# Performance work log

Measured on AMD Instinct MI355X. Metric: run time of the kernel, lower is better.

Reference implementation:

```python
import jax, jax.numpy as jnp
import numpy as np

B, S, DIN, DQ, DK = 4, 2048, 1024, 64, 64
NEG_INF = -jnp.inf


def _make_mask(sq, sk):
    # Mirrors createMask: causal mask (-inf where key_idx > query_idx),
    # except 3 randomly chosen (row, col) 'global token' pairs left at 0.
    # torch version uses random.sample; we use a fixed numpy RNG for determinism.
    rng = np.random.default_rng(0)
    g_rows = rng.choice(sk, 3, replace=False)  # sampled from range(lrlen)
    g_cols = rng.choice(sq, 3, replace=False)  # sampled from range(sequence_len)
    row = jnp.arange(sq)[:, None]
    col = jnp.arange(sk)[None, :]
    mask = jnp.where(col > row, NEG_INF, 0.0).astype(jnp.float32)
    mask = mask.at[jnp.asarray(g_rows), jnp.asarray(g_cols)].set(0.0)
    return mask  # [sq, sk]


def setup_inputs() -> dict:
    key = jax.random.key(0)
    ks = jax.random.split(key, 9)
    sc = 1.0 / np.sqrt(DIN)
    return {
        "q": jax.random.normal(ks[0], (B, S, DIN), jnp.float32),
        "k": jax.random.normal(ks[1], (B, S, DIN), jnp.float32),
        "v": jax.random.normal(ks[2], (B, S, DIN), jnp.float32),
        "Wq": jax.random.normal(ks[3], (DIN, DQ), jnp.float32) * sc,
        "bq": jax.random.normal(ks[4], (DQ,), jnp.float32) * sc,
        "Wk": jax.random.normal(ks[5], (DIN, DK), jnp.float32) * sc,
        "bk": jax.random.normal(ks[6], (DK,), jnp.float32) * sc,
        "Wv": jax.random.normal(ks[7], (DIN, DK), jnp.float32) * sc,
        "bv": jax.random.normal(ks[8], (DK,), jnp.float32) * sc,
    }


def reference(q, k, v, Wq, bq, Wk, bk, Wv, bv):
    Q = q @ Wq + bq            # [B,S,DQ]
    K = k @ Wk + bk            # [B,S,DK]
    V = v @ Wv + bv            # [B,S,DK]
    scores = jnp.einsum("bqd,bkd->bqk", Q, K)  # [B,S,S]
    mask = _make_mask(scores.shape[-2], scores.shape[-1])
    denom = jnp.asarray(K.shape[-1], jnp.float32) ** 0.5
    # NOTE: original adds mask BEFORE dividing by sqrt(d_k); -inf survives division.
    attn = jax.nn.softmax((scores + mask) / denom, axis=-1)
    return jnp.einsum("bqk,bkd->bqd", attn, V)  # [B,S,DK]
```

## Files before the change

### kernel.cpp

```cpp
#include <hip/hip_runtime.h>
#include <cstdint>
#include <cstddef>
#include <math.h>

#define SEQ    2048
#define NBATCH 4
#define DIN    1024
#define DH     64

typedef __attribute__((ext_vector_type(8))) short  short8;
typedef __attribute__((ext_vector_type(4))) float  floatx4;
typedef __attribute__((ext_vector_type(4))) unsigned short ushort4v;

#define MFMA16(a, b, c) __builtin_amdgcn_mfma_f32_16x16x32_bf16((a), (b), (c), 0, 0, 0)

__device__ __forceinline__ unsigned short f2bf(float x) {
  unsigned u = __float_as_uint(x);
  return (unsigned short)((u + 0x8000u) >> 16);
}
__device__ __forceinline__ float bf2f(unsigned short h) {
  return __uint_as_float(((unsigned)h) << 16);
}

namespace nprng {

struct PCG64 {
  __uint128_t state, inc;
  bool has_uint32;
  uint32_t uinteger;
};

static inline void pcg_step(PCG64 &g) {
  const __uint128_t MULT =
      (((__uint128_t)0x2360ed051fc65da4ULL) << 64) | 0x4385df649fccf645ULL;
  g.state = g.state * MULT + g.inc;
}

static inline uint64_t pcg_output(const PCG64 &g) {
  uint64_t hi = (uint64_t)(g.state >> 64);
  uint64_t lo = (uint64_t)g.state;
  uint64_t x = hi ^ lo;
  unsigned rot = (unsigned)(g.state >> 122) & 63u;
  return (x >> rot) | (x << ((64u - rot) & 63u));
}

static inline uint64_t pcg_next64(PCG64 &g) { pcg_step(g); return pcg_output(g); }

static inline uint32_t pcg_next32(PCG64 &g) {
  if (g.has_uint32) { g.has_uint32 = false; return g.uinteger; }
  uint64_t n = pcg_next64(g);
  g.has_uint32 = true;
  g.uinteger = (uint32_t)(n >> 32);
  return (uint32_t)(n & 0xffffffffu);
}

static inline void pcg_seed_from_seedseq0(PCG64 &g) {
  const uint32_t MULT_A = 0x931e8875u;
  const uint32_t MULT_B = 0x58f38dedu;
  const uint32_t MIX_L  = 0xca01f9ddu;
  const uint32_t MIX_R  = 0x4973f715u;
  uint32_t hc = 0x43b0d7e5u;
  uint32_t pool[4];
  for (int i = 0; i < 4; i++) {
    uint32_t v = 0u;
    v ^= hc; hc *= MULT_A; v *= hc; v ^= v >> 16;
    pool[i] = v;
  }
  for (int is = 0; is < 4; is++) {
    for (int id = 0; id < 4; id++) {
      if (is == id) continue;
      uint32_t h = pool[is];
      h ^= hc; hc *= MULT_A; h *= hc; h ^= h >> 16;
      uint32_t r = (pool[id] * MIX_L) ^ (h * MIX_R);
      r ^= r >> 16;
      pool[id] = r;
    }
  }
  uint32_t hb = 0x8b51f9ddu;
  uint32_t w[8];
  for (int i = 0; i < 8; i++) {
    uint32_t v = pool[i & 3];
    v ^= hb; hb *= MULT_B; v *= hb; v ^= v >> 16;
    w[i] = v;
  }
  uint64_t sv[4];
  for (int k = 0; k < 4; k++)
    sv[k] = (uint64_t)w[2 * k] | ((uint64_t)w[2 * k + 1] << 32);
  __uint128_t initstate = (((__uint128_t)sv[0]) << 64) | sv[1];
  __uint128_t initseq   = (((__uint128_t)sv[2]) << 64) | sv[3];
  g.state = 0; g.inc = (initseq << 1) | 1;
  pcg_step(g);
  g.state += initstate;
  pcg_step(g);
  g.has_uint32 = false; g.uinteger = 0;
}

static inline uint32_t bounded32(PCG64 &g, uint32_t rng ) {
  if (rng == 0) return 0;
  const uint32_t rng_excl = rng + 1u;
  uint64_t m = (uint64_t)pcg_next32(g) * (uint64_t)rng_excl;
  uint32_t leftover = (uint32_t)m;
  if (leftover < rng_excl) {
    const uint32_t threshold = (uint32_t)(0xffffffffu - rng) % rng_excl;
    while (leftover < threshold) {
      m = (uint64_t)pcg_next32(g) * (uint64_t)rng_excl;
      leftover = (uint32_t)m;
    }
  }
  return (uint32_t)(m >> 32);
}

static inline void choice3_2048(PCG64 &g, long long idx[3]) {
  const int pop = 2048, sz = 3;
  uint64_t hs[4] = { (uint64_t)-1, (uint64_t)-1, (uint64_t)-1, (uint64_t)-1 };
  const uint64_t mask = 3;
  for (int j = pop - sz; j < pop; j++) {
    uint64_t val = (uint64_t)bounded32(g, (uint32_t)j);
    uint64_t loc = val & mask;
    while (hs[loc] != (uint64_t)-1 && hs[loc] != val) loc = (loc + 1) & mask;
    if (hs[loc] == (uint64_t)-1) {
      hs[loc] = val;
      idx[j - pop + sz] = (long long)val;
    } else {
      loc = (uint64_t)j & mask;
      while (hs[loc] != (uint64_t)-1) loc = (loc + 1) & mask;
      hs[loc] = (uint64_t)j;
      idx[j - pop + sz] = (long long)j;
    }
  }
  for (int i = 2; i >= 1; i--) {
    uint32_t j = bounded32(g, (uint32_t)i);
    long long t = idx[j]; idx[j] = idx[i]; idx[i] = t;
  }
}

}

__global__ __launch_bounds__(256) void wtrans_kernel(
    const float* __restrict__ Wq, const float* __restrict__ Wk,
    const float* __restrict__ Wv, unsigned short* __restrict__ WT) {
  int idx = blockIdx.x * 256 + threadIdx.x;
  int p   = idx >> 16;
  int rem = idx & 65535;
  int n   = rem >> 10;
  int k   = rem & 1023;
  const float* W = (p == 0) ? Wq : (p == 1) ? Wk : Wv;
  WT[idx] = f2bf(W[k * 64 + n]);
}

__global__ __launch_bounds__(256, 3) void proj_kernel(
    const float* __restrict__ xq, const float* __restrict__ xk,
    const float* __restrict__ xv, const unsigned short* __restrict__ WT,
    const float* __restrict__ bq, const float* __restrict__ bk,
    const float* __restrict__ bv,
    unsigned short* __restrict__ QP, unsigned short* __restrict__ KP,
    unsigned short* __restrict__ VPT) {
  const int proj = blockIdx.y;
  const float* X    = (proj == 0) ? xq : (proj == 1) ? xk : xv;
  const float* bias = (proj == 0) ? bq : (proj == 1) ? bk : bv;

  const int m0   = blockIdx.x * 32;
  const int tid  = threadIdx.x;
  const int w    = tid >> 6;
  const int l    = tid & 63;
  const int quad = l >> 4;
  const int lx   = l & 15;

  __shared__ unsigned short Xs[32][264];
  __shared__ float Cs[32][68];

  const float* Xg = X + (size_t)m0 * DIN;
  const unsigned short* Wrow = WT + (size_t)proj * 65536 + (size_t)(w * 16 + lx) * 1024 + quad * 8;

  float4 xg[8];
  short8 wc[8], wn[8];

#pragma unroll
  for (int i = 0; i < 8; i++)
    xg[i] = *(const float4*)(Xg + (size_t)(4 * i + w) * DIN + l * 4);
#pragma unroll
  for (int ks = 0; ks < 8; ks++)
    wc[ks] = *(const short8*)(Wrow + ks * 32);

  floatx4 acc0 = {0.f, 0.f, 0.f, 0.f}, acc1 = acc0;

#pragma unroll
  for (int c = 0; c < 4; c++) {
#pragma unroll
    for (int i = 0; i < 8; i++) {
      ushort4v v;
      v[0] = f2bf(xg[i].x); v[1] = f2bf(xg[i].y);
      v[2] = f2bf(xg[i].z); v[3] = f2bf(xg[i].w);
      *(ushort4v*)&Xs[4 * i + w][l * 4] = v;
    }
    if (c < 3) {
      const int k0n = (c + 1) * 256;
#pragma unroll
      for (int i = 0; i < 8; i++)
        xg[i] = *(const float4*)(Xg + (size_t)(4 * i + w) * DIN + k0n + l * 4);
#pragma unroll
      for (int ks = 0; ks < 8; ks++)
        wn[ks] = *(const short8*)(Wrow + k0n + ks * 32);
    }
    __syncthreads();

#pragma unroll
    for (int ks = 0; ks < 8; ks++) {
      const short8 a0 = *(const short8*)&Xs[lx][ks * 32 + quad * 8];
      const short8 a1 = *(const short8*)&Xs[16 + lx][ks * 32 + quad * 8];
      acc0 = MFMA16(a0, wc[ks], acc0);
      acc1 = MFMA16(a1, wc[ks], acc1);
    }
    __syncthreads();

    if (c < 3) {
#pragma unroll
      for (int ks = 0; ks < 8; ks++) wc[ks] = wn[ks];
    }
  }

  const float bb = bias[w * 16 + lx];
#pragma unroll
  for (int i = 0; i < 4; i++) {
    Cs[quad * 4 + i][w * 16 + lx]      = acc0[i] + bb;
    Cs[16 + quad * 4 + i][w * 16 + lx] = acc1[i] + bb;
  }
  __syncthreads();

  if (proj < 2) {
    unsigned short* outp = (proj == 0) ? QP : KP;
    const int row = tid >> 3;
    const int d0  = (tid & 7) * 8;
    short8 v;
#pragma unroll
    for (int j = 0; j < 8; j++) v[j] = (short)f2bf(Cs[row][d0 + j]);
    *(short8*)(outp + (size_t)(m0 + row) * 64 + d0) = v;
  } else {
    const int dim = tid >> 2;
    const int s0  = (tid & 3) * 8;
    const int bq_ = m0 >> 11;
    const int sq  = (m0 & 2047) + s0;
    short8 v;
#pragma unroll
    for (int j = 0; j < 8; j++) v[j] = (short)f2bf(Cs[s0 + j][dim]);
    *(short8*)(VPT + ((size_t)bq_ * 64 + dim) * SEQ + sq) = v;
  }
}

__global__ __launch_bounds__(256, 2) void attn_kernel(
    const unsigned short* __restrict__ QP, const unsigned short* __restrict__ KP,
    const unsigned short* __restrict__ VPT, float* __restrict__ out,
    int R0, int C0, int R1, int C1, int R2, int C2) {
  const int b    = blockIdx.y;
  const int bx   = blockIdx.x;
  const int qi   = (bx & 1) ? (127 - (bx >> 1)) : (bx >> 1);
  const int q0   = qi * 16;
  const int tid  = threadIdx.x;
  const int w    = tid >> 6;
  const int l    = tid & 63;
  const int quad = l >> 4;
  const int lx   = l & 15;

  __shared__ unsigned short Ps[4][16][72];
  __shared__ float Os[4][16][64];
  __shared__ float mS[4][16], lS[4][16];
  __shared__ float lgS[3];
  __shared__ int   lgF[3];

  const unsigned short* Qb = QP + ((size_t)b * SEQ + q0) * 64;
  const unsigned short* Kb = KP + (size_t)b * SEQ * 64;
  const unsigned short* Vb = VPT + (size_t)b * 64 * SEQ;

  const short8 aq0 = *(const short8*)(Qb + (size_t)lx * 64 + quad * 8);
  const short8 aq1 = *(const short8*)(Qb + (size_t)lx * 64 + 32 + quad * 8);

  floatx4 O[4];
  float m_i[4], l_i[4];
#pragma unroll
  for (int c = 0; c < 4; c++) O[c] = (floatx4){0.f, 0.f, 0.f, 0.f};
#pragma unroll
  for (int i = 0; i < 4; i++) { m_i[i] = -INFINITY; l_i[i] = 0.f; }

  const int T = (q0 + 79) >> 6;

  for (int t = w; t < T; t += 4) {
    const int k0 = t << 6;
    const bool mT = (t == T - 1);

    short8 kf[8], vf[8];
#pragma unroll
    for (int c = 0; c < 4; c++) {
#pragma unroll
      for (int s = 0; s < 2; s++) {
        kf[c * 2 + s] = *(const short8*)(Kb + (size_t)(k0 + 16 * c + lx) * 64 + s * 32 + quad * 8);
        vf[s * 4 + c] = *(const short8*)(Vb + (size_t)(16 * c + lx) * SEQ + k0 + s * 32 + quad * 8);
      }
    }

    floatx4 sc[4];
#pragma unroll
    for (int c = 0; c < 4; c++) {
      sc[c] = (floatx4){0.f, 0.f, 0.f, 0.f};
      sc[c] = MFMA16(aq0, kf[2 * c], sc[c]);
      sc[c] = MFMA16(aq1, kf[2 * c + 1], sc[c]);
    }

    float mt[4], al[4];
#pragma unroll
    for (int i = 0; i < 4; i++) {
      const int rowg = q0 + quad * 4 + i;
      float vmax = -INFINITY;
#pragma unroll
      for (int c = 0; c < 4; c++) {
        float v = sc[c][i] * 0.125f;
        if (mT && (k0 + 16 * c + lx) > rowg) v = -INFINITY;
        sc[c][i] = v;
        vmax = fmaxf(vmax, v);
      }
      mt[i] = vmax;
    }
#pragma unroll
    for (int i = 0; i < 4; i++) {
#pragma unroll
      for (int off = 8; off >= 1; off >>= 1)
        mt[i] = fmaxf(mt[i], __shfl_xor(mt[i], off));
      const float mn = fmaxf(m_i[i], mt[i]);
      al[i] = __expf(m_i[i] - mn);
      m_i[i] = mn;
      float s = 0.f;
#pragma unroll
      for (int c = 0; c < 4; c++) {
        float p = __expf(sc[c][i] - mn);
        Ps[w][quad * 4 + i][16 * c + lx] = f2bf(p);
        s += p;
      }
#pragma unroll
      for (int off = 8; off >= 1; off >>= 1) s += __shfl_xor(s, off);
      l_i[i] = l_i[i] * al[i] + s;
    }
#pragma unroll
    for (int c = 0; c < 4; c++)
#pragma unroll
      for (int i = 0; i < 4; i++) O[c][i] *= al[i];
    asm volatile("" ::: "memory");
    const short8 pf0 = *(const short8*)&Ps[w][lx][quad * 8];
    const short8 pf1 = *(const short8*)&Ps[w][lx][32 + quad * 8];
#pragma unroll
    for (int c = 0; c < 4; c++) {
      O[c] = MFMA16(pf0, vf[c],     O[c]);
      O[c] = MFMA16(pf1, vf[4 + c], O[c]);
    }
  }

  if (lx == 0) {
#pragma unroll
    for (int i = 0; i < 4; i++) {
      mS[w][quad * 4 + i] = m_i[i];
      lS[w][quad * 4 + i] = l_i[i];
    }
  }
#pragma unroll
  for (int c = 0; c < 4; c++)
#pragma unroll
    for (int i = 0; i < 4; i++) Os[w][quad * 4 + i][16 * c + lx] = O[c][i];

  if (w == 0) {
#pragma unroll
    for (int p = 0; p < 3; p++) {
      const int R = (p == 0) ? R0 : (p == 1) ? R1 : R2;
      const int C = (p == 0) ? C0 : (p == 1) ? C1 : C2;
      const int act = (R >= q0 && R < q0 + 16 && C > R);
      float d = 0.f;
      if (act) {
        const float qv = bf2f(QP[((size_t)b * SEQ + R) * 64 + l]);
        const float kv = bf2f(KP[((size_t)b * SEQ + C) * 64 + l]);
        d = qv * kv;
#pragma unroll
        for (int off = 32; off >= 1; off >>= 1) d += __shfl_xor(d, off);
        d *= 0.125f;
      }
      if (l == 0) { lgF[p] = act; lgS[p] = d; }
    }
  }
  __syncthreads();

  {
    const int row = tid >> 4;
    const int d0  = (tid & 15) * 4;
    const int Rs[3] = {R0, R1, R2};
    const int Cs3[3] = {C0, C1, C2};

    float mf = -INFINITY;
#pragma unroll
    for (int w4 = 0; w4 < 4; w4++) mf = fmaxf(mf, mS[w4][row]);
#pragma unroll
    for (int p = 0; p < 3; p++)
      if (lgF[p] && (Rs[p] - q0) == row) mf = fmaxf(mf, lgS[p]);

    float lf = 0.f;
    float o0 = 0.f, o1 = 0.f, o2 = 0.f, o3 = 0.f;
#pragma unroll
    for (int w4 = 0; w4 < 4; w4++) {
      const float a = __expf(mS[w4][row] - mf);
      lf += a * lS[w4][row];
      const float* op = &Os[w4][row][d0];
      o0 += a * op[0]; o1 += a * op[1]; o2 += a * op[2]; o3 += a * op[3];
    }
#pragma unroll
    for (int p = 0; p < 3; p++) {
      if (lgF[p] && (Rs[p] - q0) == row) {
        const float pe = __expf(lgS[p] - mf);
        lf += pe;
        const int C = Cs3[p];
        o0 += pe * bf2f(Vb[(size_t)(d0 + 0) * SEQ + C]);
        o1 += pe * bf2f(Vb[(size_t)(d0 + 1) * SEQ + C]);
        o2 += pe * bf2f(Vb[(size_t)(d0 + 2) * SEQ + C]);
        o3 += pe * bf2f(Vb[(size_t)(d0 + 3) * SEQ + C]);
      }
    }
    const float inv = 1.0f / lf;
    float4 r;
    r.x = o0 * inv; r.y = o1 * inv; r.z = o2 * inv; r.w = o3 * inv;
    *(float4*)(out + ((size_t)b * SEQ + q0 + row) * 64 + d0) = r;
  }
}

extern "C" void kernel_launch(void* const* d_in, const int* in_sizes, int n_in,
                              void* d_out, int out_size, void* d_ws,
                              size_t ws_size, hipStream_t stream) {
  const float* xq = (const float*)d_in[0];
  const float* xk = (const float*)d_in[1];
  const float* xv = (const float*)d_in[2];
  const float* Wq = (const float*)d_in[3];
  const float* bq = (const float*)d_in[4];
  const float* Wk = (const float*)d_in[5];
  const float* bk = (const float*)d_in[6];
  const float* Wv = (const float*)d_in[7];
  const float* bv = (const float*)d_in[8];
  float* out = (float*)d_out;

  unsigned short* QP  = (unsigned short*)d_ws;
  unsigned short* KP  = QP + (size_t)NBATCH * SEQ * 64;
  unsigned short* VPT = KP + (size_t)NBATCH * SEQ * 64;
  unsigned short* WT  = VPT + (size_t)NBATCH * 64 * SEQ;

  nprng::PCG64 g;
  nprng::pcg_seed_from_seedseq0(g);
  long long rows[3], cols[3];
  nprng::choice3_2048(g, rows);
  nprng::choice3_2048(g, cols);

  wtrans_kernel<<<768, 256, 0, stream>>>(Wq, Wk, Wv, WT);

  dim3 pgrid(256, 3);
  proj_kernel<<<pgrid, 256, 0, stream>>>(xq, xk, xv, WT, bq, bk, bv, QP, KP, VPT);

  dim3 agrid(SEQ / 16, NBATCH);
  attn_kernel<<<agrid, 256, 0, stream>>>(
      QP, KP, VPT, out, (int)rows[0], (int)cols[0], (int)rows[1], (int)cols[1],
      (int)rows[2], (int)cols[2]);
}
```

Measured before the change: 175.6 us.

## Stage projection X and W tiles in LDS via async global_load_lds

```diff
diff --git a/kernel.cpp b/kernel.cpp
--- a/kernel.cpp
+++ b/kernel.cpp
@@ -20,6 +20,17 @@
 }
 __device__ __forceinline__ float bf2f(unsigned short h) {
   return __uint_as_float(((unsigned)h) << 16);
+}
+
+__device__ __forceinline__ void async_cp4(const void* g, void* l) {
+  __builtin_amdgcn_global_load_lds(
+      (const __attribute__((address_space(1))) void*)g,
+      (__attribute__((address_space(3))) void*)l, 4, 0, 0);
+}
+__device__ __forceinline__ void async_cp16(const void* g, void* l) {
+  __builtin_amdgcn_global_load_lds(
+      (const __attribute__((address_space(1))) void*)g,
+      (__attribute__((address_space(3))) void*)l, 16, 0, 0);
 }
 
 namespace nprng {
@@ -138,92 +149,86 @@
 
 __global__ __launch_bounds__(256) void wtrans_kernel(
     const float* __restrict__ Wq, const float* __restrict__ Wk,
-    const float* __restrict__ Wv, unsigned short* __restrict__ WT) {
+    const float* __restrict__ Wv, unsigned short* __restrict__ WTc) {
   int idx = blockIdx.x * 256 + threadIdx.x;
   int p   = idx >> 16;
   int rem = idx & 65535;
   int n   = rem >> 10;
   int k   = rem & 1023;
   const float* W = (p == 0) ? Wq : (p == 1) ? Wk : Wv;
-  WT[idx] = f2bf(W[k * 64 + n]);
+  unsigned short v = f2bf(W[k * 64 + n]);
+  int dst = ((p * 8 + (k >> 7)) * 64 + n) * 128 + (k & 127);
+  WTc[dst] = v;
 }
 
 __global__ __launch_bounds__(256, 3) void proj_kernel(
     const float* __restrict__ xq, const float* __restrict__ xk,
-    const float* __restrict__ xv, const unsigned short* __restrict__ WT,
+    const float* __restrict__ xv, const unsigned short* __restrict__ WTc,
     const float* __restrict__ bq, const float* __restrict__ bk,
     const float* __restrict__ bv,
     unsigned short* __restrict__ QP, unsigned short* __restrict__ KP,
     unsigned short* __restrict__ VPT) {
-  const int proj = blockIdx.y;
+  const int m0g  = blockIdx.x * 32;
+  const int proj = m0g >> 13;
+  const int m0   = m0g & 8191;
   const float* X    = (proj == 0) ? xq : (proj == 1) ? xk : xv;
   const float* bias = (proj == 0) ? bq : (proj == 1) ? bk : bv;
 
-  const int m0   = blockIdx.x * 32;
   const int tid  = threadIdx.x;
   const int w    = tid >> 6;
   const int l    = tid & 63;
   const int quad = l >> 4;
   const int lx   = l & 15;
-
-  __shared__ unsigned short Xs[32][264];
-  __shared__ float Cs[32][68];
-
-  const float* Xg = X + (size_t)m0 * DIN;
-  const unsigned short* Wrow = WT + (size_t)proj * 65536 + (size_t)(w * 16 + lx) * 1024 + quad * 8;
-
-  float4 xg[8];
-  short8 wc[8], wn[8];
-
-#pragma unroll
-  for (int i = 0; i < 8; i++)
-    xg[i] = *(const float4*)(Xg + (size_t)(4 * i + w) * DIN + l * 4);
-#pragma unroll
-  for (int ks = 0; ks < 8; ks++)
-    wc[ks] = *(const short8*)(Wrow + ks * 32);
+  const int mr   = (w & 1) * 16;
+  const int nc   = (w >> 1) * 32;
+
+  __shared__ float          Xs[32 * 132];
+  __shared__ unsigned short Ws[16 * 520];
+  __shared__ float          Cs[32][68];
+
+  const float* Xblk = X + (size_t)m0 * DIN;
+  const unsigned short* Wpj = WTc + (size_t)proj * 8 * 8192;
 
   floatx4 acc0 = {0.f, 0.f, 0.f, 0.f}, acc1 = acc0;
 
-#pragma unroll
-  for (int c = 0; c < 4; c++) {
+  for (int kc = 0; kc < 8; kc++) {
 #pragma unroll
     for (int i = 0; i < 8; i++) {
-      ushort4v v;
-      v[0] = f2bf(xg[i].x); v[1] = f2bf(xg[i].y);
-      v[2] = f2bf(xg[i].z); v[3] = f2bf(xg[i].w);
-      *(ushort4v*)&Xs[4 * i + w][l * 4] = v;
-    }
-    if (c < 3) {
-      const int k0n = (c + 1) * 256;
-#pragma unroll
-      for (int i = 0; i < 8; i++)
-        xg[i] = *(const float4*)(Xg + (size_t)(4 * i + w) * DIN + k0n + l * 4);
-#pragma unroll
-      for (int ks = 0; ks < 8; ks++)
-        wn[ks] = *(const short8*)(Wrow + k0n + ks * 32);
+      const int r = 8 * w + i;
+      const float* g = Xblk + (size_t)r * DIN + kc * 128;
+      async_cp4(g + l,      &Xs[r * 132]);
+      async_cp4(g + 64 + l, &Xs[r * 132 + 64]);
+    }
+#pragma unroll
+    for (int i = 0; i < 4; i++) {
+      const int g4 = 4 * w + i;
+      const unsigned short* gsrc = Wpj + (size_t)kc * 8192 + g4 * 512;
+      async_cp16((const char*)gsrc + l * 16, &Ws[g4 * 520]);
     }
     __syncthreads();
 
 #pragma unroll
-    for (int ks = 0; ks < 8; ks++) {
-      const short8 a0 = *(const short8*)&Xs[lx][ks * 32 + quad * 8];
-      const short8 a1 = *(const short8*)&Xs[16 + lx][ks * 32 + quad * 8];
-      acc0 = MFMA16(a0, wc[ks], acc0);
-      acc1 = MFMA16(a1, wc[ks], acc1);
+    for (int ks = 0; ks < 4; ks++) {
+      const float* ap = &Xs[(mr + lx) * 132 + ks * 32 + quad * 8];
+      const float4 f0 = *(const float4*)ap;
+      const float4 f1 = *(const float4*)(ap + 4);
+      short8 a;
+      a[0] = f2bf(f0.x); a[1] = f2bf(f0.y); a[2] = f2bf(f0.z); a[3] = f2bf(f0.w);
+      a[4] = f2bf(f1.x); a[5] = f2bf(f1.y); a[6] = f2bf(f1.z); a[7] = f2bf(f1.w);
+      const int c0 = nc + lx, c1 = nc + 16 + lx;
+      const short8 b0 = *(const short8*)&Ws[(c0 >> 2) * 520 + (c0 & 3) * 128 + ks * 32 + quad * 8];
+      const short8 b1 = *(const short8*)&Ws[(c1 >> 2) * 520 + (c1 & 3) * 128 + ks * 32 + quad * 8];
+      acc0 = MFMA16(a, b0, acc0);
+      acc1 = MFMA16(a, b1, acc1);
     }
     __syncthreads();
-
-    if (c < 3) {
-#pragma unroll
-      for (int ks = 0; ks < 8; ks++) wc[ks] = wn[ks];
-    }
-  }
-
-  const float bb = bias[w * 16 + lx];
+  }
+
+  const float bb0 = bias[nc + lx], bb1 = bias[nc + 16 + lx];
 #pragma unroll
   for (int i = 0; i < 4; i++) {
-    Cs[quad * 4 + i][w * 16 + lx]      = acc0[i] + bb;
-    Cs[16 + quad * 4 + i][w * 16 + lx] = acc1[i] + bb;
+    Cs[mr + quad * 4 + i][nc + lx]      = acc0[i] + bb0;
+    Cs[mr + quad * 4 + i][nc + 16 + lx] = acc1[i] + bb1;
   }
   __syncthreads();
 
@@ -442,7 +447,7 @@
   unsigned short* QP  = (unsigned short*)d_ws;
   unsigned short* KP  = QP + (size_t)NBATCH * SEQ * 64;
   unsigned short* VPT = KP + (size_t)NBATCH * SEQ * 64;
-  unsigned short* WT  = VPT + (size_t)NBATCH * 64 * SEQ;
+  unsigned short* WTc = VPT + (size_t)NBATCH * 64 * SEQ;
 
   nprng::PCG64 g;
   nprng::pcg_seed_from_seedseq0(g);
@@ -450,10 +455,9 @@
   nprng::choice3_2048(g, rows);
   nprng::choice3_2048(g, cols);
 
-  wtrans_kernel<<<768, 256, 0, stream>>>(Wq, Wk, Wv, WT);
-
-  dim3 pgrid(256, 3);
-  proj_kernel<<<pgrid, 256, 0, stream>>>(xq, xk, xv, WT, bq, bk, bv, QP, KP, VPT);
+  wtrans_kernel<<<768, 256, 0, stream>>>(Wq, Wk, Wv, WTc);
+
+  proj_kernel<<<768, 256, 0, stream>>>(xq, xk, xv, WTc, bq, bk, bv, QP, KP, VPT);
 
   dim3 agrid(SEQ / 16, NBATCH);
   attn_kernel<<<agrid, 256, 0, stream>>>(
```

After: 168.7 us. 4.0% less time.
